# Kernel optimization log

Hardware: AMD Instinct MI355X
Metric: run time of the kernel (lower is better)

## Reference

```python
import jax, jax.numpy as jnp
import numpy as np

D = 128; H = 8; DH = D // H
N = 50000; B = 8; MAXN = N // B
E = 400000
NG_G = 4; NG_L = 4; NG = NG_G + NG_L
DFF = 2 * D


def _ln(x, eps=1e-5):
    m = x.mean(-1, keepdims=True)
    v = ((x - m) ** 2).mean(-1, keepdims=True)
    return (x - m) * jax.lax.rsqrt(v + eps)


def _mha(q, k, v, in_w, in_b, out_w, out_b):
    # torch nn.MultiheadAttention (batch_first, eval) with packed in_proj
    Bq, Lq, d = q.shape; Lk = k.shape[1]
    wq, wk, wv = jnp.split(in_w, 3, axis=0)
    bq, bk, bv = jnp.split(in_b, 3)
    Q = (q @ wq.T + bq).reshape(Bq, Lq, H, DH).transpose(0, 2, 1, 3)
    K = (k @ wk.T + bk).reshape(Bq, Lk, H, DH).transpose(0, 2, 1, 3)
    V = (v @ wv.T + bv).reshape(Bq, Lk, H, DH).transpose(0, 2, 1, 3)
    A = jax.nn.softmax(jnp.einsum('bhqd,bhkd->bhqk', Q, K) / np.float32(np.sqrt(DH)), axis=-1)
    O = jnp.einsum('bhqk,bhkd->bhqd', A, V).transpose(0, 2, 1, 3).reshape(Bq, Lq, d)
    return O @ out_w.T + out_b, A.mean(axis=1)  # averaged attn weights over heads


def _tconv(x, src, dst, Wq, bq, Wk, bk, Wv, bv, Wskip, bskip, Wbeta):
    # PyG TransformerConv(d, d//H, heads=H, beta=True): edge-wise gather-attend-scatter
    n = x.shape[0]
    q = (x @ Wq.T + bq)[dst].reshape(-1, H, DH)   # [E,H,DH] query at target node
    k = (x @ Wk.T + bk)[src].reshape(-1, H, DH)
    v = (x @ Wv.T + bv)[src].reshape(-1, H, DH)
    logits = (q * k).sum(-1) / np.float32(np.sqrt(DH))  # [E,H]
    m = jax.ops.segment_max(logits, dst, num_segments=n)
    m = jnp.where(jnp.isfinite(m), m, 0.0)
    a = jnp.exp(logits - m[dst])
    s = jax.ops.segment_sum(a, dst, num_segments=n)
    alpha = a / (s[dst] + 1e-16)                  # per-target-node softmax (PyG softmax)
    out = jax.ops.segment_sum(v * alpha[..., None], dst, num_segments=n).reshape(n, D)
    xr = x @ Wskip.T + bskip                      # root weight
    beta = jax.nn.sigmoid(jnp.concatenate([out, xr, out - xr], axis=-1) @ Wbeta.T)
    return beta * xr + (1.0 - beta) * out


def setup_inputs() -> dict:
    key = jax.random.key(0)
    ks = jax.random.split(key, 16)
    w = lambda i, shape, s=0.05: jax.random.normal(ks[i], shape, jnp.float32) * s
    return dict(
        x=w(0, (N, D), 1.0),
        edge_index=jax.random.randint(ks[1], (2, E), 0, N),
        global_h=w(2, (B, NG, D), 1.0),
        batch=jnp.repeat(jnp.arange(B, dtype=jnp.int32), MAXN),  # sorted, even split
        n_global_tokens_global=NG_G,
        n_global_tokens_local=NG_L,
        Wq=w(3, (D, D)), bq=jnp.zeros((D,), jnp.float32),
        Wk=w(4, (D, D)), bk=jnp.zeros((D,), jnp.float32),
        Wv=w(5, (D, D)), bv=jnp.zeros((D,), jnp.float32),
        Wskip=w(6, (D, D)), bskip=jnp.zeros((D,), jnp.float32),
        Wbeta=w(7, (1, 3 * D)),
        ng_in_w=w(8, (3 * D, D)), ng_in_b=jnp.zeros((3 * D,), jnp.float32),
        ng_out_w=w(9, (D, D)), ng_out_b=jnp.zeros((D,), jnp.float32),
        gn_in_w=w(10, (3 * D, D)), gn_in_b=jnp.zeros((3 * D,), jnp.float32),
        gn_out_w=w(11, (D, D)), gn_out_b=jnp.zeros((D,), jnp.float32),
        W1=w(12, (DFF, D)), b1=jnp.zeros((DFF,), jnp.float32),
        W2=w(13, (D, DFF)), b2=jnp.zeros((D,), jnp.float32),
    )


def reference(x, edge_index, global_h, batch, n_global_tokens_global, n_global_tokens_local,
              Wq, bq, Wk, bk, Wv, bv, Wskip, bskip, Wbeta,
              ng_in_w, ng_in_b, ng_out_w, ng_out_b,
              gn_in_w, gn_in_b, gn_out_w, gn_out_b,
              W1, b1, W2, b2):
    src, dst = edge_index[0], edge_index[1]
    h_local = _tconv(x, src, dst, Wq, bq, Wk, bk, Wv, bv, Wskip, bskip, Wbeta)
    x = _ln(x + h_local)
    Bg = global_h.shape[0]
    # to_dense_batch: batch is sorted with equal-size graphs -> mask all True, pure reshape
    dense_x = x.reshape(Bg, -1, D)
    global_out, attn_w = _mha(global_h, dense_x, dense_x, ng_in_w, ng_in_b, ng_out_w, ng_out_b)
    global_h = _ln(global_h + global_out)
    nodes_out, _ = _mha(dense_x, global_h, global_h, gn_in_w, gn_in_b, gn_out_w, gn_out_b)
    dense_x = _ln(dense_x + nodes_out)
    x = dense_x.reshape(-1, D)  # un-scatter (even split -> reshape)
    ff = jax.nn.relu(x @ W1.T + b1) @ W2.T + b2
    x = _ln(x + ff)
    # attention regularization, vectorized over the per-graph python loop
    ls = n_global_tokens_global
    le = ls + n_global_tokens_local
    P = attn_w[:, ls:le, :]                      # [B, K, max_n], all nodes valid
    Pn = P / (P.sum(-1, keepdims=True) + 1e-8)
    G = jnp.einsum('bkn,bmn->bkm', Pn, Pn)       # [B, K, K]
    Kt = le - ls
    off = (G.sum(axis=(1, 2)) - jnp.einsum('bkk->b', G)) / (Kt * Kt - Kt)
    reg = off.mean()
    return x, global_h, reg
```

## Files before the change

kernel.cpp:

```cpp
#include <hip/hip_runtime.h>
#include <math.h>

#define D 128
#define H 8
#define NGT 8
#define LSTOK 4
#define NCH 4

typedef short bf16x8 __attribute__((ext_vector_type(8)));
typedef float f32x4  __attribute__((ext_vector_type(4)));

__device__ __forceinline__ short f2bf(float f) {
  union { float f; unsigned u; } v; v.f = f;
  unsigned r = v.u + 0x7FFFu + ((v.u >> 16) & 1u);
  return (short)(r >> 16);
}
__device__ __forceinline__ float bf2f(short s) {
  union { unsigned u; float f; } v;
  v.u = ((unsigned)(unsigned short)s) << 16;
  return v.f;
}
__device__ __forceinline__ float4 bf4(bf16x8 v, int lo) {
  return make_float4(bf2f(v[lo]), bf2f(v[lo + 1]), bf2f(v[lo + 2]), bf2f(v[lo + 3]));
}
__device__ __forceinline__ unsigned pk2(float a, float b) {
  return ((unsigned)(unsigned short)f2bf(b) << 16) | (unsigned short)f2bf(a);
}

__device__ __forceinline__ float dot4(float4 a, float4 b) {
  return a.x*b.x + a.y*b.y + a.z*b.z + a.w*b.w;
}
__device__ __forceinline__ float4 scale_madd(float4 a, float sc, float4 v, float p) {
  return make_float4(fmaf(p, v.x, a.x*sc), fmaf(p, v.y, a.y*sc),
                     fmaf(p, v.z, a.z*sc), fmaf(p, v.w, a.w*sc));
}
__device__ __forceinline__ float4 comb4(float4 a, float e1, float4 c, float e2) {
  return make_float4(a.x*e1 + c.x*e2, a.y*e1 + c.y*e2, a.z*e1 + c.z*e2, a.w*e1 + c.w*e2);
}
__device__ __forceinline__ float4 shfl_xor4(float4 v, int off) {
  return make_float4(__shfl_xor(v.x, off), __shfl_xor(v.y, off),
                     __shfl_xor(v.z, off), __shfl_xor(v.w, off));
}

struct CvtArgs {
  const float* s[10];
  short*       d[10];
  int          n[10];
};

__global__ void cvt_weights(CvtArgs a) {
  int which = blockIdx.y;
  const float* s = a.s[which];
  short* d = a.d[which];
  int n = a.n[which];
  int i = (blockIdx.x * 256 + threadIdx.x) * 4;
  if (i + 3 < n) {
    float4 v = *(const float4*)(s + i);
    d[i]     = f2bf(v.x);
    d[i + 1] = f2bf(v.y);
    d[i + 2] = f2bf(v.z);
    d[i + 3] = f2bf(v.w);
  }
}

__global__ void cvt_x(const float* __restrict__ s, short* __restrict__ d, int n) {
  int i = (blockIdx.x * 256 + threadIdx.x) * 8;
  if (i + 7 < n) {
    float4 a = *(const float4*)(s + i);
    float4 b = *(const float4*)(s + i + 4);
    bf16x8 v;
    v[0] = f2bf(a.x); v[1] = f2bf(a.y); v[2] = f2bf(a.z); v[3] = f2bf(a.w);
    v[4] = f2bf(b.x); v[5] = f2bf(b.y); v[6] = f2bf(b.z); v[7] = f2bf(b.w);
    *(bf16x8*)(d + i) = v;
  }
}

__global__ void concat_bias4(const float* __restrict__ b0, const float* __restrict__ b1,
                             const float* __restrict__ b2, const float* __restrict__ b3,
                             float* __restrict__ out) {
  int t = threadIdx.x;
  out[t] = b0[t]; out[128 + t] = b1[t]; out[256 + t] = b2[t]; out[384 + t] = b3[t];
}

#define EPST 72
template<int K>
__global__ void __launch_bounds__(256) gemm_direct(const short* __restrict__ A,
    const short* __restrict__ Wb, const float* __restrict__ bias,
    short* __restrict__ out16, int C16, int s16,
    float* __restrict__ out32, int s32,
    int Nrows, int Ccols, int relu)
{
  __shared__ short eplds[4][64 * EPST];
  const int t = threadIdx.x;
  const int wid = t >> 6, lane = t & 63;
  const int rowBase = blockIdx.x * 128 + (wid >> 1) * 64;
  const int colBase = blockIdx.y * 128 + (wid & 1) * 64;
  const int lrow = lane & 15;
  const int lk = (lane >> 4) * 8;

  f32x4 acc[4][4];
  f32x4 z4 = {0.f, 0.f, 0.f, 0.f};
#pragma unroll
  for (int m = 0; m < 4; m++)
#pragma unroll
    for (int n = 0; n < 4; n++) acc[m][n] = z4;

  const short* ap[4];
#pragma unroll
  for (int m = 0; m < 4; ++m) {
    int ar = rowBase + m * 16 + lrow;
    if (ar >= Nrows) ar = Nrows - 1;
    ap[m] = A + (size_t)ar * K + lk;
  }
  const short* wp[4];
#pragma unroll
  for (int n = 0; n < 4; ++n)
    wp[n] = Wb + (size_t)(colBase + n * 16 + lrow) * K + lk;

#pragma unroll
  for (int kb = 0; kb < K; kb += 32) {
    bf16x8 af[4], bfr[4];
#pragma unroll
    for (int m = 0; m < 4; ++m) af[m] = *(const bf16x8*)(ap[m] + kb);
#pragma unroll
    for (int n = 0; n < 4; ++n) bfr[n] = *(const bf16x8*)(wp[n] + kb);
#pragma unroll
    for (int m = 0; m < 4; ++m)
#pragma unroll
      for (int n = 0; n < 4; ++n)
        acc[m][n] = __builtin_amdgcn_mfma_f32_16x16x32_bf16(af[m], bfr[n], acc[m][n], 0, 0, 0);
  }

  const int ccol = lane & 15;
  const int rquad = (lane >> 4) * 4;
  if (colBase < C16) {
    short* lds = eplds[wid];
#pragma unroll
    for (int n = 0; n < 4; ++n) {
      float bb = bias[colBase + n * 16 + ccol];
      int col = n * 16 + ccol;
#pragma unroll
      for (int m = 0; m < 4; ++m) {
        int r0 = m * 16 + rquad;
#pragma unroll
        for (int r = 0; r < 4; ++r) {
          float v = acc[m][n][r] + bb;
          if (relu) v = fmaxf(v, 0.f);
          lds[(r0 + r) * EPST + col] = f2bf(v);
        }
      }
    }
    const int jr = lane >> 3, jc = lane & 7;
#pragma unroll
    for (int i = 0; i < 8; ++i) {
      int row = i * 8 + jr;
      int gr = rowBase + row;
      if (gr < Nrows) {
        bf16x8 v = *(const bf16x8*)(lds + row * EPST + jc * 8);
        *(bf16x8*)(out16 + (size_t)gr * s16 + colBase + jc * 8) = v;
      }
    }
  } else {
#pragma unroll
    for (int n = 0; n < 4; ++n) {
      int col = colBase + n * 16 + ccol;
      float bb = bias[col];
#pragma unroll
      for (int m = 0; m < 4; ++m) {
        int row0 = rowBase + m * 16 + rquad;
#pragma unroll
        for (int r = 0; r < 4; ++r) {
          int gr = row0 + r;
          if (gr < Nrows) {
            float v = acc[m][n][r] + bb;
            if (relu) v = fmaxf(v, 0.f);
            out32[(size_t)gr * s32 + (col - C16)] = v;
          }
        }
      }
    }
  }
}

__global__ void gemm_small(const float* __restrict__ A, const float* __restrict__ W,
                           const float* __restrict__ bias, float* __restrict__ out, int M)
{
  int r = blockIdx.x;
  int c = threadIdx.x;
  __shared__ float as[128];
  as[c] = A[(size_t)r * 128 + c];
  __syncthreads();
  float acc = bias[c];
  const float* wr = W + (size_t)c * 128;
#pragma unroll 4
  for (int k = 0; k < 128; k++) acc += as[k] * wr[k];
  out[(size_t)r * 128 + c] = acc;
}

__global__ void count_deg(const int* __restrict__ dst, int* __restrict__ deg, int E) {
  int e = blockIdx.x * 256 + threadIdx.x;
  if (e < E) atomicAdd(&deg[dst[e]], 1);
}

__global__ void scan_pass1(const int* __restrict__ deg, int* __restrict__ bsum, int N) {
  int t = threadIdx.x, lane = t & 63, wid = t >> 6;
  int idx = blockIdx.x * 1024 + t * 4;
  int4 v = {0, 0, 0, 0};
  if (idx + 3 < N) v = *(const int4*)(deg + idx);
  else {
    if (idx < N) v.x = deg[idx];
    if (idx + 1 < N) v.y = deg[idx + 1];
    if (idx + 2 < N) v.z = deg[idx + 2];
    if (idx + 3 < N) v.w = deg[idx + 3];
  }
  int s = v.x + v.y + v.z + v.w;
#pragma unroll
  for (int off = 32; off >= 1; off >>= 1) s += __shfl_xor(s, off);
  __shared__ int ws[4];
  if (lane == 0) ws[wid] = s;
  __syncthreads();
  if (t == 0) bsum[blockIdx.x] = ws[0] + ws[1] + ws[2] + ws[3];
}

__global__ void scan_pass2(int* __restrict__ bsum, int SB) {
  __shared__ int sh[1024];
  int t = threadIdx.x;
  sh[t] = (t < SB) ? bsum[t] : 0;
  __syncthreads();
  for (int off = 1; off < 1024; off <<= 1) {
    int v = (t >= off) ? sh[t - off] : 0;
    __syncthreads();
    sh[t] += v;
    __syncthreads();
  }
  if (t < SB) bsum[t] = (t == 0) ? 0 : sh[t - 1];
}

__global__ void scan_pass3(const int* __restrict__ deg, const int* __restrict__ bsum,
                           int* __restrict__ row_start, int* __restrict__ cursor,
                           int N, int E)
{
  int t = threadIdx.x, lane = t & 63, wid = t >> 6;
  int idx = blockIdx.x * 1024 + t * 4;
  int4 v = {0, 0, 0, 0};
  if (idx + 3 < N) v = *(const int4*)(deg + idx);
  else {
    if (idx < N) v.x = deg[idx];
    if (idx + 1 < N) v.y = deg[idx + 1];
    if (idx + 2 < N) v.z = deg[idx + 2];
    if (idx + 3 < N) v.w = deg[idx + 3];
  }
  int ts = v.x + v.y + v.z + v.w;
  int x = ts;
#pragma unroll
  for (int off = 1; off < 64; off <<= 1) {
    int y = __shfl_up(x, off);
    if (lane >= off) x += y;
  }
  __shared__ int ws[4];
  if (lane == 63) ws[wid] = x;
  __syncthreads();
  int woff = 0;
  for (int i = 0; i < wid; i++) woff += ws[i];
  int p = bsum[blockIdx.x] + woff + (x - ts);
  if (idx < N)     { row_start[idx] = p; cursor[idx] = p; }     p += v.x;
  if (idx + 1 < N) { row_start[idx + 1] = p; cursor[idx + 1] = p; } p += v.y;
  if (idx + 2 < N) { row_start[idx + 2] = p; cursor[idx + 2] = p; } p += v.z;
  if (idx + 3 < N) { row_start[idx + 3] = p; cursor[idx + 3] = p; }
  if (blockIdx.x == 0 && t == 0) row_start[N] = E;
}

__global__ void fill_edges(const int* __restrict__ dst, const int* __restrict__ src,
                           int* __restrict__ cursor, int* __restrict__ edge_src, int E) {
  int e = blockIdx.x * 256 + threadIdx.x;
  if (e < E) {
    int p = atomicAdd(&cursor[dst[e]], 1);
    edge_src[p] = src[e];
  }
}

__global__ void tconv_attn(const short* __restrict__ qkvb,
                           const int* __restrict__ row_start,
                           const int* __restrict__ edge_src,
                           float* __restrict__ out, int N)
{
  int gid = blockIdx.x * 256 + threadIdx.x;
  if (gid >= N * H) return;
  int n = gid >> 3, h = gid & 7;
  const short* qp = qkvb + (size_t)n * 384 + h * 16;
  bf16x8 qa = *(const bf16x8*)(qp);
  bf16x8 qb = *(const bf16x8*)(qp + 8);
  float4 q0 = bf4(qa, 0), q1 = bf4(qa, 4), q2 = bf4(qb, 0), q3 = bf4(qb, 4);
  int e0 = row_start[n], e1 = row_start[n + 1];

  float mA = -3.0e38f, sA = 0.f;
  float4 A0 = make_float4(0, 0, 0, 0), A1 = A0, A2 = A0, A3 = A0;
  float mB = -3.0e38f, sB = 0.f;
  float4 B0 = A0, B1 = A0, B2 = A0, B3 = A0;

  int ei = e0;
  for (; ei + 1 < e1; ei += 2) {
    int sn0 = edge_src[ei], sn1 = edge_src[ei + 1];
    const short* kp0 = qkvb + (size_t)sn0 * 384 + 128 + h * 16;
    const short* kp1 = qkvb + (size_t)sn1 * 384 + 128 + h * 16;
    bf16x8 k00 = *(const bf16x8*)(kp0);
    bf16x8 k01 = *(const bf16x8*)(kp0 + 8);
    bf16x8 k10 = *(const bf16x8*)(kp1);
    bf16x8 k11 = *(const bf16x8*)(kp1 + 8);
    float d0 = (dot4(q0, bf4(k00, 0)) + dot4(q1, bf4(k00, 4))
              + dot4(q2, bf4(k01, 0)) + dot4(q3, bf4(k01, 4))) * 0.25f;
    float d1 = (dot4(q0, bf4(k10, 0)) + dot4(q1, bf4(k10, 4))
              + dot4(q2, bf4(k11, 0)) + dot4(q3, bf4(k11, 4))) * 0.25f;
    bf16x8 v00 = *(const bf16x8*)(kp0 + 128);
    bf16x8 v01 = *(const bf16x8*)(kp0 + 136);
    bf16x8 v10 = *(const bf16x8*)(kp1 + 128);
    bf16x8 v11 = *(const bf16x8*)(kp1 + 136);
    float mn0 = fmaxf(mA, d0);
    float sc0 = expf(mA - mn0), p0 = expf(d0 - mn0);
    A0 = scale_madd(A0, sc0, bf4(v00, 0), p0);
    A1 = scale_madd(A1, sc0, bf4(v00, 4), p0);
    A2 = scale_madd(A2, sc0, bf4(v01, 0), p0);
    A3 = scale_madd(A3, sc0, bf4(v01, 4), p0);
    sA = sA * sc0 + p0; mA = mn0;
    float mn1 = fmaxf(mB, d1);
    float sc1 = expf(mB - mn1), p1 = expf(d1 - mn1);
    B0 = scale_madd(B0, sc1, bf4(v10, 0), p1);
    B1 = scale_madd(B1, sc1, bf4(v10, 4), p1);
    B2 = scale_madd(B2, sc1, bf4(v11, 0), p1);
    B3 = scale_madd(B3, sc1, bf4(v11, 4), p1);
    sB = sB * sc1 + p1; mB = mn1;
  }
  if (ei < e1) {
    int sn0 = edge_src[ei];
    const short* kp0 = qkvb + (size_t)sn0 * 384 + 128 + h * 16;
    bf16x8 k00 = *(const bf16x8*)(kp0);
    bf16x8 k01 = *(const bf16x8*)(kp0 + 8);
    float d0 = (dot4(q0, bf4(k00, 0)) + dot4(q1, bf4(k00, 4))
              + dot4(q2, bf4(k01, 0)) + dot4(q3, bf4(k01, 4))) * 0.25f;
    bf16x8 v00 = *(const bf16x8*)(kp0 + 128);
    bf16x8 v01 = *(const bf16x8*)(kp0 + 136);
    float mn0 = fmaxf(mA, d0);
    float sc0 = expf(mA - mn0), p0 = expf(d0 - mn0);
    A0 = scale_madd(A0, sc0, bf4(v00, 0), p0);
    A1 = scale_madd(A1, sc0, bf4(v00, 4), p0);
    A2 = scale_madd(A2, sc0, bf4(v01, 0), p0);
    A3 = scale_madd(A3, sc0, bf4(v01, 4), p0);
    sA = sA * sc0 + p0; mA = mn0;
  }
  float mn = fmaxf(mA, mB);
  float eA = expf(mA - mn), eB = expf(mB - mn);
  float s = sA * eA + sB * eB;
  float4 a0 = comb4(A0, eA, B0, eB);
  float4 a1 = comb4(A1, eA, B1, eB);
  float4 a2 = comb4(A2, eA, B2, eB);
  float4 a3 = comb4(A3, eA, B3, eB);
  float inv = 1.f / (s + 1e-16f);
  float4* o4 = (float4*)(out + (size_t)n * 128 + h * 16);
  o4[0] = make_float4(a0.x * inv, a0.y * inv, a0.z * inv, a0.w * inv);
  o4[1] = make_float4(a1.x * inv, a1.y * inv, a1.z * inv, a1.w * inv);
  o4[2] = make_float4(a2.x * inv, a2.y * inv, a2.z * inv, a2.w * inv);
  o4[3] = make_float4(a3.x * inv, a3.y * inv, a3.z * inv, a3.w * inv);
}

__global__ void gate_ln(const float* __restrict__ x, const float* __restrict__ att,
                        const float* __restrict__ xr32, const float* __restrict__ Wb,
                        float* __restrict__ x1, short* __restrict__ x1b, int N)
{
  int wid = threadIdx.x >> 6, lane = threadIdx.x & 63;
  int n = blockIdx.x * 4 + wid;
  if (n >= N) return;
  size_t base = (size_t)n * 128 + lane * 2;
  float2 o = *(const float2*)(att + base);
  float2 r = *(const float2*)(xr32 + base);
  float2 xv = *(const float2*)(x + base);
  float2 w0 = *(const float2*)(Wb + lane * 2);
  float2 w1 = *(const float2*)(Wb + 128 + lane * 2);
  float2 w2 = *(const float2*)(Wb + 256 + lane * 2);
  float ts = o.x * w0.x + o.y * w0.y + r.x * w1.x + r.y * w1.y
           + (o.x - r.x) * w2.x + (o.y - r.y) * w2.y;
#pragma unroll
  for (int mm = 32; mm >= 1; mm >>= 1) ts += __shfl_xor(ts, mm);
  float beta = 1.f / (1.f + expf(-ts));
  float2 y;
  y.x = xv.x + beta * r.x + (1.f - beta) * o.x;
  y.y = xv.y + beta * r.y + (1.f - beta) * o.y;
  float sm = y.x + y.y;
#pragma unroll
  for (int mm = 32; mm >= 1; mm >>= 1) sm += __shfl_xor(sm, mm);
  float mean = sm * (1.f / 128.f);
  float dx = y.x - mean, dy = y.y - mean;
  float vs = dx * dx + dy * dy;
#pragma unroll
  for (int mm = 32; mm >= 1; mm >>= 1) vs += __shfl_xor(vs, mm);
  float rstd = rsqrtf(vs * (1.f / 128.f) + 1e-5f);
  float ox = dx * rstd, oy = dy * rstd;
  *(float2*)(x1 + base) = make_float2(ox, oy);
  *(unsigned*)(x1b + base) = pk2(ox, oy);
}

__global__ void ln_add(const float* __restrict__ a, const float* __restrict__ b,
                       float* __restrict__ out, short* __restrict__ out16, int R)
{
  int wid = threadIdx.x >> 6, lane = threadIdx.x & 63;
  int r = blockIdx.x * 4 + wid;
  if (r >= R) return;
  size_t base = (size_t)r * 128 + lane * 2;
  float2 av = *(const float2*)(a + base);
  float2 bv = *(const float2*)(b + base);
  float2 y = make_float2(av.x + bv.x, av.y + bv.y);
  float sm = y.x + y.y;
#pragma unroll
  for (int mm = 32; mm >= 1; mm >>= 1) sm += __shfl_xor(sm, mm);
  float mean = sm * (1.f / 128.f);
  float dx = y.x - mean, dy = y.y - mean;
  float vs = dx * dx + dy * dy;
#pragma unroll
  for (int mm = 32; mm >= 1; mm >>= 1) vs += __shfl_xor(vs, mm);
  float rstd = rsqrtf(vs * (1.f / 128.f) + 1e-5f);
  float ox = dx * rstd, oy = dy * rstd;
  *(float2*)(out + base) = make_float2(ox, oy);
  if (out16) *(unsigned*)(out16 + base) = pk2(ox, oy);
}

__global__ void glob_part(const float* __restrict__ Qg, const short* __restrict__ kv,
                          float* __restrict__ Plog,
                          float* __restrict__ pm, float* __restrict__ ps,
                          float* __restrict__ pacc, int MAXN)
{
  int blk = blockIdx.x;
  int ch = blockIdx.y;
  int h = blk & 7, g = (blk >> 3) & 7, b = blk >> 6;
  int lane = threadIdx.x;
  const float4* q4 = (const float4*)(Qg + (size_t)(b * NGT + g) * 128 + h * 16);
  float4 q0 = q4[0], q1 = q4[1], q2 = q4[2], q3 = q4[3];
  int chunk = (MAXN + NCH - 1) / NCH;
  int n0 = ch * chunk;
  int n1 = n0 + chunk; if (n1 > MAXN) n1 = MAXN;
  float* plrow = (g >= LSTOK) ? Plog + (((size_t)(b * 4 + g - LSTOK)) * H + h) * MAXN : nullptr;
  float m = -3.0e38f, s = 0.f;
  float4 a0 = make_float4(0, 0, 0, 0), a1 = a0, a2 = a0, a3 = a0;
  for (int n = n0 + lane; n < n1; n += 64) {
    const short* kp = kv + ((size_t)(b * MAXN + n)) * 256 + h * 16;
    bf16x8 k0 = *(const bf16x8*)(kp);
    bf16x8 k1 = *(const bf16x8*)(kp + 8);
    float d = dot4(q0, bf4(k0, 0)) + dot4(q1, bf4(k0, 4))
            + dot4(q2, bf4(k1, 0)) + dot4(q3, bf4(k1, 4));
    d *= 0.25f;
    if (plrow) plrow[n] = d;
    float mn = fmaxf(m, d);
    float sc = expf(m - mn);
    float p = expf(d - mn);
    bf16x8 v0 = *(const bf16x8*)(kp + 128);
    bf16x8 v1 = *(const bf16x8*)(kp + 136);
    a0 = scale_madd(a0, sc, bf4(v0, 0), p);
    a1 = scale_madd(a1, sc, bf4(v0, 4), p);
    a2 = scale_madd(a2, sc, bf4(v1, 0), p);
    a3 = scale_madd(a3, sc, bf4(v1, 4), p);
    s = s * sc + p;
    m = mn;
  }
#pragma unroll
  for (int off = 32; off >= 1; off >>= 1) {
    float m2 = __shfl_xor(m, off);
    float s2 = __shfl_xor(s, off);
    float4 c0 = shfl_xor4(a0, off), c1 = shfl_xor4(a1, off);
    float4 c2 = shfl_xor4(a2, off), c3 = shfl_xor4(a3, off);
    float mn = fmaxf(m, m2);
    float e1 = expf(m - mn), e2 = expf(m2 - mn);
    s = s * e1 + s2 * e2;
    a0 = comb4(a0, e1, c0, e2);
    a1 = comb4(a1, e1, c1, e2);
    a2 = comb4(a2, e1, c2, e2);
    a3 = comb4(a3, e1, c3, e2);
    m = mn;
  }
  if (lane == 0) {
    int pi = blk * NCH + ch;
    pm[pi] = m; ps[pi] = s;
    float4* pa = (float4*)(pacc + (size_t)pi * 16);
    pa[0] = a0; pa[1] = a1; pa[2] = a2; pa[3] = a3;
  }
}

__global__ void glob_merge(const float* __restrict__ pm, const float* __restrict__ ps,
                           const float* __restrict__ pacc, float* __restrict__ Og,
                           float* __restrict__ m_gl, float* __restrict__ is_gl)
{
  int blk = blockIdx.x;
  int lane = threadIdx.x;
  float m = -3.0e38f;
#pragma unroll
  for (int c = 0; c < NCH; ++c) m = fmaxf(m, pm[blk * NCH + c]);
  float s = 0.f;
#pragma unroll
  for (int c = 0; c < NCH; ++c) s += ps[blk * NCH + c] * expf(pm[blk * NCH + c] - m);
  if (lane < 16) {
    float a = 0.f;
#pragma unroll
    for (int c = 0; c < NCH; ++c)
      a += pacc[(size_t)(blk * NCH + c) * 16 + lane] * expf(pm[blk * NCH + c] - m);
    int h = blk & 7, g = (blk >> 3) & 7, b = blk >> 6;
    Og[(size_t)(b * NGT + g) * 128 + h * 16 + lane] = a / s;
  }
  if (lane == 0) { m_gl[blk] = m; is_gl[blk] = 1.f / s; }
}

__global__ void pker2(const float* __restrict__ Plog,
                      const float* __restrict__ m_gl, const float* __restrict__ is_gl,
                      float* __restrict__ P, int MAXN)
{
  int b = blockIdx.y;
  __shared__ float ms[32], iss[32];
  if (threadIdx.x < 32) {
    int g = threadIdx.x >> 3, h = threadIdx.x & 7;
    ms[threadIdx.x]  = m_gl[(b * NGT + LSTOK + g) * H + h];
    iss[threadIdx.x] = is_gl[(b * NGT + LSTOK + g) * H + h];
  }
  __syncthreads();
  int n = blockIdx.x * 256 + threadIdx.x;
  if (n >= MAXN) return;
#pragma unroll
  for (int g = 0; g < 4; g++) {
    float acc = 0.f;
#pragma unroll
    for (int h = 0; h < H; h++) {
      float l = Plog[(((size_t)(b * 4 + g)) * H + h) * MAXN + n];
      acc += expf(l - ms[g * 8 + h]) * iss[g * 8 + h];
    }
    P[(size_t)(b * 4 + g) * MAXN + n] = acc * 0.125f;
  }
}

__global__ void regk(const float* __restrict__ P, float* __restrict__ offb, int MAXN)
{
  int b = blockIdx.x;
  int t = threadIdx.x;
  float v[10];
#pragma unroll
  for (int i = 0; i < 10; i++) v[i] = 0.f;
  for (int n = t; n < MAXN; n += 256) {
    float p0 = P[(size_t)(b * 4 + 0) * MAXN + n];
    float p1 = P[(size_t)(b * 4 + 1) * MAXN + n];
    float p2 = P[(size_t)(b * 4 + 2) * MAXN + n];
    float p3 = P[(size_t)(b * 4 + 3) * MAXN + n];
    v[0] += p0; v[1] += p1; v[2] += p2; v[3] += p3;
    v[4] += p0 * p1; v[5] += p0 * p2; v[6] += p0 * p3;
    v[7] += p1 * p2; v[8] += p1 * p3; v[9] += p2 * p3;
  }
#pragma unroll
  for (int i = 0; i < 10; i++) {
    float x = v[i];
#pragma unroll
    for (int mm = 32; mm >= 1; mm >>= 1) x += __shfl_xor(x, mm);
    v[i] = x;
  }
  __shared__ float red[4][10];
  int wid = t >> 6, lane = t & 63;
  if (lane == 0)
    for (int i = 0; i < 10; i++) red[wid][i] = v[i];
  __syncthreads();
  if (t == 0) {
    float r[10];
    for (int i = 0; i < 10; i++) r[i] = red[0][i] + red[1][i] + red[2][i] + red[3][i];
    float r0 = r[0] + 1e-8f, r1 = r[1] + 1e-8f, r2 = r[2] + 1e-8f, r3 = r[3] + 1e-8f;
    float off = 2.f * (r[4] / (r0 * r1) + r[5] / (r0 * r2) + r[6] / (r0 * r3)
                     + r[7] / (r1 * r2) + r[8] / (r1 * r3) + r[9] / (r2 * r3));
    offb[b] = off * (1.f / 12.f);
  }
}

__global__ void regfin(const float* __restrict__ offb, float* __restrict__ out) {
  if (threadIdx.x == 0 && blockIdx.x == 0) {
    float s = 0.f;
    for (int i = 0; i < 8; i++) s += offb[i];
    *out = s * (1.f / 8.f);
  }
}

__global__ void node_attn(const short* __restrict__ Qn, const float* __restrict__ Kg,
                          const float* __restrict__ Vg, short* __restrict__ On,
                          int N, int MAXN)
{
  __shared__ float kg[2][NGT * 128];
  __shared__ float vg[2][NGT * 128];
  int n0 = blockIdx.x * 32;
  int b0 = n0 / MAXN;
  int nlast = n0 + 31; if (nlast >= N) nlast = N - 1;
  int bLast = nlast / MAXN;
  int nb = (bLast != b0) ? 2 : 1;
  for (int bi = 0; bi < nb; ++bi) {
    size_t gb = (size_t)((b0 + bi) * NGT) * 128;
    int i = threadIdx.x * 4;
    *(float4*)&kg[bi][i] = *(const float4*)(Kg + gb + i);
    *(float4*)&vg[bi][i] = *(const float4*)(Vg + gb + i);
  }
  __syncthreads();
  int n = n0 + (threadIdx.x >> 3), h = threadIdx.x & 7;
  if (n >= N) return;
  int bi = (n / MAXN) - b0;
  const short* qp = Qn + (size_t)n * 128 + h * 16;
  bf16x8 qa = *(const bf16x8*)(qp);
  bf16x8 qb = *(const bf16x8*)(qp + 8);
  float4 q0 = bf4(qa, 0), q1 = bf4(qa, 4), q2 = bf4(qb, 0), q3 = bf4(qb, 4);
  float l[NGT];
  float mx = -3.0e38f;
#pragma unroll
  for (int tk = 0; tk < NGT; tk++) {
    const float4* k4 = (const float4*)(&kg[bi][tk * 128 + h * 16]);
    float d = dot4(q0, k4[0]) + dot4(q1, k4[1]) + dot4(q2, k4[2]) + dot4(q3, k4[3]);
    l[tk] = d * 0.25f;
    mx = fmaxf(mx, l[tk]);
  }
  float s = 0.f;
#pragma unroll
  for (int tk = 0; tk < NGT; tk++) { l[tk] = expf(l[tk] - mx); s += l[tk]; }
  float inv = 1.f / s;
  float4 a0 = make_float4(0, 0, 0, 0), a1 = a0, a2 = a0, a3 = a0;
#pragma unroll
  for (int tk = 0; tk < NGT; tk++) {
    float p = l[tk] * inv;
    const float4* v4 = (const float4*)(&vg[bi][tk * 128 + h * 16]);
    a0 = scale_madd(a0, 1.f, v4[0], p);
    a1 = scale_madd(a1, 1.f, v4[1], p);
    a2 = scale_madd(a2, 1.f, v4[2], p);
    a3 = scale_madd(a3, 1.f, v4[3], p);
  }
  unsigned* o = (unsigned*)(On + (size_t)n * 128 + h * 16);
  o[0] = pk2(a0.x, a0.y); o[1] = pk2(a0.z, a0.w);
  o[2] = pk2(a1.x, a1.y); o[3] = pk2(a1.z, a1.w);
  o[4] = pk2(a2.x, a2.y); o[5] = pk2(a2.z, a2.w);
  o[6] = pk2(a3.x, a3.y); o[7] = pk2(a3.z, a3.w);
}

extern "C" void kernel_launch(void* const* d_in, const int* in_sizes, int n_in,
                              void* d_out, int out_size, void* d_ws, size_t ws_size,
                              hipStream_t stream)
{
  const float* x     = (const float*)d_in[0];
  const int*   ei    = (const int*)d_in[1];
  const float* gh    = (const float*)d_in[2];
  const float* Wq    = (const float*)d_in[6];
  const float* bqv   = (const float*)d_in[7];
  const float* Wk    = (const float*)d_in[8];
  const float* bkv   = (const float*)d_in[9];
  const float* Wv    = (const float*)d_in[10];
  const float* bvv   = (const float*)d_in[11];
  const float* Wsk   = (const float*)d_in[12];
  const float* bsk   = (const float*)d_in[13];
  const float* Wbeta = (const float*)d_in[14];
  const float* ngw   = (const float*)d_in[15];
  const float* ngb   = (const float*)d_in[16];
  const float* ngow  = (const float*)d_in[17];
  const float* ngob  = (const float*)d_in[18];
  const float* gnw   = (const float*)d_in[19];
  const float* gnb   = (const float*)d_in[20];
  const float* gnow  = (const float*)d_in[21];
  const float* gnob  = (const float*)d_in[22];
  const float* W1    = (const float*)d_in[23];
  const float* b1v   = (const float*)d_in[24];
  const float* W2    = (const float*)d_in[25];
  const float* b2v   = (const float*)d_in[26];

  const int N    = in_sizes[0] / D;
  const int E    = in_sizes[1] / 2;
  const int Bb   = 8;
  const int MAXN = N / Bb;

  const int* srcI = ei;
  const int* dstI = ei + E;

  size_t NF = (size_t)N;
  size_t ND = NF * D;
  float* fw = (float*)d_ws;
  short* qkvb = (short*)fw;
  short* kv16 = qkvb;
  short* ff1b = qkvb;
  float* xr32 = fw + NF * 192;
  short* Qnb  = (short*)xr32;
  short* Onb  = (short*)(xr32 + NF * 64);
  float* ff2o = xr32;
  float* x1   = fw + NF * 320;
  short* x1b  = (short*)(fw + NF * 448);
  float* misc = fw + NF * 512;
  float* Qg    = misc;
  float* Og    = Qg + 8192;
  float* gout  = Og + 8192;
  float* Kg    = gout + 8192;
  float* Vg    = Kg + 8192;
  float* m_gl  = Vg + 8192;
  float* is_gl = m_gl + 512;
  float* Pbuf  = is_gl + 512;
  float* offb  = Pbuf + (size_t)Bb * 4 * MAXN;
  float* bias512 = offb + 16;
  float* Plog  = bias512 + 512;
  float* pm    = Plog + (size_t)4 * H * Bb * MAXN;
  float* ps    = pm + 512 * NCH;
  float* pacc  = ps + 512 * NCH;
  int* deg       = (int*)(pacc + 512 * NCH * 16);
  int* row_start = deg + N;
  int* cursor    = row_start + N + 1;
  int* bsum      = cursor + N;
  int* edge_src  = bsum + 1024;
  short* wbase = (short*)((((uintptr_t)(edge_src + E)) + 15) & ~(uintptr_t)15);
  short* cWq  = wbase;
  short* cWk  = cWq  + 16384;
  short* cWv  = cWk  + 16384;
  short* cWsk = cWv  + 16384;
  short* cNgK = cWsk + 16384;
  short* cNgV = cNgK + 16384;
  short* cGnQ = cNgV + 16384;
  short* cGnO = cGnQ + 16384;
  short* cW1  = cGnO + 16384;
  short* cW2  = cW1  + 32768;
  short* xb   = cW2  + 32768;

  float* outx   = (float*)d_out;
  float* outgh  = outx + ND;
  float* outreg = outgh + (size_t)Bb * NGT * D;
  float* wa     = outx;

  const int GXM = (N + 127) / 128;
  const int SB  = (N + 1023) / 1024;
  dim3 blk256(256);

  CvtArgs ca;
  ca.s[0] = Wq;   ca.d[0] = cWq;  ca.n[0] = 16384;
  ca.s[1] = Wk;   ca.d[1] = cWk;  ca.n[1] = 16384;
  ca.s[2] = Wv;   ca.d[2] = cWv;  ca.n[2] = 16384;
  ca.s[3] = Wsk;  ca.d[3] = cWsk; ca.n[3] = 16384;
  ca.s[4] = ngw + 128 * 128; ca.d[4] = cNgK; ca.n[4] = 16384;
  ca.s[5] = ngw + 256 * 128; ca.d[5] = cNgV; ca.n[5] = 16384;
  ca.s[6] = gnw;  ca.d[6] = cGnQ; ca.n[6] = 16384;
  ca.s[7] = gnow; ca.d[7] = cGnO; ca.n[7] = 16384;
  ca.s[8] = W1;   ca.d[8] = cW1;  ca.n[8] = 32768;
  ca.s[9] = W2;   ca.d[9] = cW2;  ca.n[9] = 32768;
  cvt_weights<<<dim3(32, 10), blk256, 0, stream>>>(ca);
  concat_bias4<<<dim3(1), dim3(128), 0, stream>>>(bqv, bkv, bvv, bsk, bias512);
  cvt_x<<<dim3((N * 128 / 8 + 255) / 256), blk256, 0, stream>>>(x, xb, N * 128);

  hipMemsetAsync(deg, 0, (size_t)N * sizeof(int), stream);
  count_deg<<<dim3((E + 255) / 256), blk256, 0, stream>>>(dstI, deg, E);
  scan_pass1<<<dim3(SB), blk256, 0, stream>>>(deg, bsum, N);
  scan_pass2<<<dim3(1), dim3(1024), 0, stream>>>(bsum, SB);
  scan_pass3<<<dim3(SB), blk256, 0, stream>>>(deg, bsum, row_start, cursor, N, E);
  fill_edges<<<dim3((E + 255) / 256), blk256, 0, stream>>>(dstI, srcI, cursor, edge_src, E);

  gemm_direct<128><<<dim3(GXM, 4), blk256, 0, stream>>>(xb, cWq, bias512,
                                                        qkvb, 384, 384, xr32, 128,
                                                        N, 512, 0);

  tconv_attn<<<dim3((N * H + 255) / 256), blk256, 0, stream>>>(qkvb, row_start, edge_src, wa, N);
  gate_ln<<<dim3((N + 3) / 4), blk256, 0, stream>>>(x, wa, xr32, Wbeta, x1, x1b, N);

  gemm_direct<128><<<dim3(GXM, 2), blk256, 0, stream>>>(x1b, cNgK, ngb + 128,
                                                        kv16, 256, 256, nullptr, 0,
                                                        N, 256, 0);
  gemm_small<<<dim3(64), dim3(128), 0, stream>>>(gh, ngw, ngb, Qg, 64);
  glob_part<<<dim3(512, NCH), dim3(64), 0, stream>>>(Qg, kv16, Plog, pm, ps, pacc, MAXN);
  glob_merge<<<dim3(512), dim3(64), 0, stream>>>(pm, ps, pacc, Og, m_gl, is_gl);
  pker2<<<dim3((MAXN + 255) / 256, 8), blk256, 0, stream>>>(Plog, m_gl, is_gl, Pbuf, MAXN);
  regk<<<dim3(8), blk256, 0, stream>>>(Pbuf, offb, MAXN);
  regfin<<<dim3(1), dim3(64), 0, stream>>>(offb, outreg);

  gemm_small<<<dim3(64), dim3(128), 0, stream>>>(Og, ngow, ngob, gout, 64);
  ln_add<<<dim3(16), blk256, 0, stream>>>(gh, gout, outgh, nullptr, 64);

  gemm_small<<<dim3(64), dim3(128), 0, stream>>>(outgh, gnw + 128 * 128, gnb + 128, Kg, 64);
  gemm_small<<<dim3(64), dim3(128), 0, stream>>>(outgh, gnw + 256 * 128, gnb + 256, Vg, 64);
  gemm_direct<128><<<dim3(GXM, 1), blk256, 0, stream>>>(x1b, cGnQ, gnb,
                                                        Qnb, 128, 128, nullptr, 0,
                                                        N, 128, 0);
  node_attn<<<dim3((N + 31) / 32), blk256, 0, stream>>>(Qnb, Kg, Vg, Onb, N, MAXN);
  gemm_direct<128><<<dim3(GXM, 1), blk256, 0, stream>>>(Onb, cGnO, gnob,
                                                        nullptr, 0, 0, wa, 128,
                                                        N, 128, 0);
  ln_add<<<dim3((N + 3) / 4), blk256, 0, stream>>>(x1, wa, x1, x1b, N);

  gemm_direct<128><<<dim3(GXM, 2), blk256, 0, stream>>>(x1b, cW1, b1v,
                                                        ff1b, 256, 256, nullptr, 0,
                                                        N, 256, 1);
  gemm_direct<256><<<dim3(GXM, 1), blk256, 0, stream>>>(ff1b, cW2, b2v,
                                                        nullptr, 0, 0, ff2o, 128,
                                                        N, 128, 0);
  ln_add<<<dim3((N + 3) / 4), blk256, 0, stream>>>(x1, ff2o, outx, nullptr, N);
}
```

Before: 394.6 us.

## Fuse FFN GEMMs and node-attention pipeline into single LDS-staged kernels

Adds gemm_ff, which computes the relu hidden layer of the feed-forward block into shared memory as bf16 and runs the second GEMM from there, so the 256-wide intermediate never goes to global memory. Adds gemm_node, which fuses the Q projection, the per-node attention over the 8 global tokens, and the output projection in one kernel with Q and the attention output held in LDS. The QKV GEMM now writes the skip projection as bf16 in a 512-wide packed buffer, and gate_ln reads it from there instead of a separate fp32 buffer. Together these cut launches and global round-trips, at the cost of large LDS use per block (about 66 KB in gemm_ff), which lowers occupancy, and bf16 rounding of the skip term.

New measurement: 361.3 us, median of 2. 8.4% less time.

```diff
diff --git a/kernel.cpp b/kernel.cpp
--- a/kernel.cpp
+++ b/kernel.cpp
@@ -182,6 +182,276 @@
   }
 }
 
+#define FFST 264
+__global__ void __launch_bounds__(256) gemm_ff(const short* __restrict__ A,
+    const short* __restrict__ W1b, const float* __restrict__ b1,
+    const short* __restrict__ W2b, const float* __restrict__ b2,
+    float* __restrict__ out, int Nrows)
+{
+  __shared__ short flds[128 * FFST];
+  const int t = threadIdx.x;
+  const int wid = t >> 6, lane = t & 63;
+  const int rowL = (wid >> 1) * 64;
+  const int rowBase = blockIdx.x * 128 + rowL;
+  const int lrow = lane & 15;
+  const int lk = (lane >> 4) * 8;
+  const int ccol = lane & 15;
+  const int rquad = (lane >> 4) * 4;
+  f32x4 z4 = {0.f, 0.f, 0.f, 0.f};
+
+  const short* ap[4];
+#pragma unroll
+  for (int m = 0; m < 4; ++m) {
+    int ar = rowBase + m * 16 + lrow;
+    if (ar >= Nrows) ar = Nrows - 1;
+    ap[m] = A + (size_t)ar * 128 + lk;
+  }
+
+  for (int cb = 0; cb < 2; ++cb) {
+    int colBase = cb * 128 + (wid & 1) * 64;
+    f32x4 acc[4][4];
+#pragma unroll
+    for (int m = 0; m < 4; m++)
+#pragma unroll
+      for (int n = 0; n < 4; n++) acc[m][n] = z4;
+    const short* wp[4];
+#pragma unroll
+    for (int n = 0; n < 4; ++n)
+      wp[n] = W1b + (size_t)(colBase + n * 16 + lrow) * 128 + lk;
+#pragma unroll
+    for (int kb = 0; kb < 128; kb += 32) {
+      bf16x8 af[4], bfr[4];
+#pragma unroll
+      for (int m = 0; m < 4; ++m) af[m] = *(const bf16x8*)(ap[m] + kb);
+#pragma unroll
+      for (int n = 0; n < 4; ++n) bfr[n] = *(const bf16x8*)(wp[n] + kb);
+#pragma unroll
+      for (int m = 0; m < 4; ++m)
+#pragma unroll
+        for (int n = 0; n < 4; ++n)
+          acc[m][n] = __builtin_amdgcn_mfma_f32_16x16x32_bf16(af[m], bfr[n], acc[m][n], 0, 0, 0);
+    }
+#pragma unroll
+    for (int n = 0; n < 4; ++n) {
+      int col = colBase + n * 16 + ccol;
+      float bb = b1[col];
+#pragma unroll
+      for (int m = 0; m < 4; ++m) {
+        int r0 = rowL + m * 16 + rquad;
+#pragma unroll
+        for (int r = 0; r < 4; ++r) {
+          float v = fmaxf(acc[m][n][r] + bb, 0.f);
+          flds[(r0 + r) * FFST + col] = f2bf(v);
+        }
+      }
+    }
+  }
+  __syncthreads();
+
+  {
+    int colBase = (wid & 1) * 64;
+    f32x4 acc[4][4];
+#pragma unroll
+    for (int m = 0; m < 4; m++)
+#pragma unroll
+      for (int n = 0; n < 4; n++) acc[m][n] = z4;
+    const short* wp[4];
+#pragma unroll
+    for (int n = 0; n < 4; ++n)
+      wp[n] = W2b + (size_t)(colBase + n * 16 + lrow) * 256 + lk;
+#pragma unroll
+    for (int kb = 0; kb < 256; kb += 32) {
+      bf16x8 af[4], bfr[4];
+#pragma unroll
+      for (int m = 0; m < 4; ++m)
+        af[m] = *(const bf16x8*)(flds + (rowL + m * 16 + lrow) * FFST + kb + lk);
+#pragma unroll
+      for (int n = 0; n < 4; ++n) bfr[n] = *(const bf16x8*)(wp[n] + kb);
+#pragma unroll
+      for (int m = 0; m < 4; ++m)
+#pragma unroll
+        for (int n = 0; n < 4; ++n)
+          acc[m][n] = __builtin_amdgcn_mfma_f32_16x16x32_bf16(af[m], bfr[n], acc[m][n], 0, 0, 0);
+    }
+#pragma unroll
+    for (int n = 0; n < 4; ++n) {
+      int col = colBase + n * 16 + ccol;
+      float bb = b2[col];
+#pragma unroll
+      for (int m = 0; m < 4; ++m) {
+        int row0 = rowBase + m * 16 + rquad;
+#pragma unroll
+        for (int r = 0; r < 4; ++r) {
+          int gr = row0 + r;
+          if (gr < Nrows) out[(size_t)gr * 128 + col] = acc[m][n][r] + bb;
+        }
+      }
+    }
+  }
+}
+
+#define QST 136
+__global__ void __launch_bounds__(256) gemm_node(const short* __restrict__ A,
+    const short* __restrict__ GnQb, const float* __restrict__ gnbq,
+    const float* __restrict__ Kg, const float* __restrict__ Vg,
+    const short* __restrict__ GnOb, const float* __restrict__ gnbo,
+    float* __restrict__ out, int Nrows, int MAXN)
+{
+  __shared__ short qlds[128 * QST];
+  __shared__ float kg[2][NGT * 128];
+  __shared__ float vg[2][NGT * 128];
+  const int t = threadIdx.x;
+  const int wid = t >> 6, lane = t & 63;
+  const int rowL = (wid >> 1) * 64;
+  const int n0 = blockIdx.x * 128;
+  const int rowBase = n0 + rowL;
+  const int colBase = (wid & 1) * 64;
+  const int lrow = lane & 15;
+  const int lk = (lane >> 4) * 8;
+  const int ccol = lane & 15;
+  const int rquad = (lane >> 4) * 4;
+  f32x4 z4 = {0.f, 0.f, 0.f, 0.f};
+
+  int b0 = n0 / MAXN;
+  int nlast = n0 + 127; if (nlast >= Nrows) nlast = Nrows - 1;
+  int bLast = nlast / MAXN;
+  int nb = (bLast != b0) ? 2 : 1;
+  for (int bi = 0; bi < nb; ++bi) {
+    size_t gb = (size_t)((b0 + bi) * NGT) * 128;
+    int i = t * 4;
+    *(float4*)&kg[bi][i] = *(const float4*)(Kg + gb + i);
+    *(float4*)&vg[bi][i] = *(const float4*)(Vg + gb + i);
+  }
+
+  {
+    f32x4 acc[4][4];
+#pragma unroll
+    for (int m = 0; m < 4; m++)
+#pragma unroll
+      for (int n = 0; n < 4; n++) acc[m][n] = z4;
+    const short* ap[4];
+#pragma unroll
+    for (int m = 0; m < 4; ++m) {
+      int ar = rowBase + m * 16 + lrow;
+      if (ar >= Nrows) ar = Nrows - 1;
+      ap[m] = A + (size_t)ar * 128 + lk;
+    }
+    const short* wp[4];
+#pragma unroll
+    for (int n = 0; n < 4; ++n)
+      wp[n] = GnQb + (size_t)(colBase + n * 16 + lrow) * 128 + lk;
+#pragma unroll
+    for (int kb = 0; kb < 128; kb += 32) {
+      bf16x8 af[4], bfr[4];
+#pragma unroll
+      for (int m = 0; m < 4; ++m) af[m] = *(const bf16x8*)(ap[m] + kb);
+#pragma unroll
+      for (int n = 0; n < 4; ++n) bfr[n] = *(const bf16x8*)(wp[n] + kb);
+#pragma unroll
+      for (int m = 0; m < 4; ++m)
+#pragma unroll
+        for (int n = 0; n < 4; ++n)
+          acc[m][n] = __builtin_amdgcn_mfma_f32_16x16x32_bf16(af[m], bfr[n], acc[m][n], 0, 0, 0);
+    }
+#pragma unroll
+    for (int n = 0; n < 4; ++n) {
+      int col = colBase + n * 16 + ccol;
+      float bb = gnbq[col];
+#pragma unroll
+      for (int m = 0; m < 4; ++m) {
+        int r0 = rowL + m * 16 + rquad;
+#pragma unroll
+        for (int r = 0; r < 4; ++r)
+          qlds[(r0 + r) * QST + col] = f2bf(acc[m][n][r] + bb);
+      }
+    }
+  }
+  __syncthreads();
+
+#pragma unroll
+  for (int u = 0; u < 4; ++u) {
+    int unit = t + u * 256;
+    int row = unit >> 3, h = unit & 7;
+    int grow = n0 + row;
+    if (grow < Nrows) {
+      int bi = (grow / MAXN) - b0;
+      short* qp = qlds + row * QST + h * 16;
+      bf16x8 qa = *(const bf16x8*)(qp);
+      bf16x8 qb = *(const bf16x8*)(qp + 8);
+      float4 q0 = bf4(qa, 0), q1 = bf4(qa, 4), q2 = bf4(qb, 0), q3 = bf4(qb, 4);
+      float l[NGT];
+      float mx = -3.0e38f;
+#pragma unroll
+      for (int tk = 0; tk < NGT; tk++) {
+        const float4* k4 = (const float4*)(&kg[bi][tk * 128 + h * 16]);
+        float d = dot4(q0, k4[0]) + dot4(q1, k4[1]) + dot4(q2, k4[2]) + dot4(q3, k4[3]);
+        l[tk] = d * 0.25f;
+        mx = fmaxf(mx, l[tk]);
+      }
+      float s = 0.f;
+#pragma unroll
+      for (int tk = 0; tk < NGT; tk++) { l[tk] = expf(l[tk] - mx); s += l[tk]; }
+      float inv = 1.f / s;
+      float4 a0 = make_float4(0, 0, 0, 0), a1 = a0, a2 = a0, a3 = a0;
+#pragma unroll
+      for (int tk = 0; tk < NGT; tk++) {
+        float p = l[tk] * inv;
+        const float4* v4 = (const float4*)(&vg[bi][tk * 128 + h * 16]);
+        a0 = scale_madd(a0, 1.f, v4[0], p);
+        a1 = scale_madd(a1, 1.f, v4[1], p);
+        a2 = scale_madd(a2, 1.f, v4[2], p);
+        a3 = scale_madd(a3, 1.f, v4[3], p);
+      }
+      unsigned* o = (unsigned*)qp;
+      o[0] = pk2(a0.x, a0.y); o[1] = pk2(a0.z, a0.w);
+      o[2] = pk2(a1.x, a1.y); o[3] = pk2(a1.z, a1.w);
+      o[4] = pk2(a2.x, a2.y); o[5] = pk2(a2.z, a2.w);
+      o[6] = pk2(a3.x, a3.y); o[7] = pk2(a3.z, a3.w);
+    }
+  }
+  __syncthreads();
+
+  {
+    f32x4 acc[4][4];
+#pragma unroll
+    for (int m = 0; m < 4; m++)
+#pragma unroll
+      for (int n = 0; n < 4; n++) acc[m][n] = z4;
+    const short* wp[4];
+#pragma unroll
+    for (int n = 0; n < 4; ++n)
+      wp[n] = GnOb + (size_t)(colBase + n * 16 + lrow) * 128 + lk;
+#pragma unroll
+    for (int kb = 0; kb < 128; kb += 32) {
+      bf16x8 af[4], bfr[4];
+#pragma unroll
+      for (int m = 0; m < 4; ++m)
+        af[m] = *(const bf16x8*)(qlds + (rowL + m * 16 + lrow) * QST + kb + lk);
+#pragma unroll
+      for (int n = 0; n < 4; ++n) bfr[n] = *(const bf16x8*)(wp[n] + kb);
+#pragma unroll
+      for (int m = 0; m < 4; ++m)
+#pragma unroll
+        for (int n = 0; n < 4; ++n)
+          acc[m][n] = __builtin_amdgcn_mfma_f32_16x16x32_bf16(af[m], bfr[n], acc[m][n], 0, 0, 0);
+    }
+#pragma unroll
+    for (int n = 0; n < 4; ++n) {
+      int col = colBase + n * 16 + ccol;
+      float bb = gnbo[col];
+#pragma unroll
+      for (int m = 0; m < 4; ++m) {
+        int row0 = rowBase + m * 16 + rquad;
+#pragma unroll
+        for (int r = 0; r < 4; ++r) {
+          int gr = row0 + r;
+          if (gr < Nrows) out[(size_t)gr * 128 + col] = acc[m][n][r] + bb;
+        }
+      }
+    }
+  }
+}
+
 __global__ void gemm_small(const float* __restrict__ A, const float* __restrict__ W,
                            const float* __restrict__ bias, float* __restrict__ out, int M)
 {
@@ -287,7 +557,7 @@
   int gid = blockIdx.x * 256 + threadIdx.x;
   if (gid >= N * H) return;
   int n = gid >> 3, h = gid & 7;
-  const short* qp = qkvb + (size_t)n * 384 + h * 16;
+  const short* qp = qkvb + (size_t)n * 512 + h * 16;
   bf16x8 qa = *(const bf16x8*)(qp);
   bf16x8 qb = *(const bf16x8*)(qp + 8);
   float4 q0 = bf4(qa, 0), q1 = bf4(qa, 4), q2 = bf4(qb, 0), q3 = bf4(qb, 4);
@@ -301,8 +571,8 @@
   int ei = e0;
   for (; ei + 1 < e1; ei += 2) {
     int sn0 = edge_src[ei], sn1 = edge_src[ei + 1];
-    const short* kp0 = qkvb + (size_t)sn0 * 384 + 128 + h * 16;
-    const short* kp1 = qkvb + (size_t)sn1 * 384 + 128 + h * 16;
+    const short* kp0 = qkvb + (size_t)sn0 * 512 + 128 + h * 16;
+    const short* kp1 = qkvb + (size_t)sn1 * 512 + 128 + h * 16;
     bf16x8 k00 = *(const bf16x8*)(kp0);
     bf16x8 k01 = *(const bf16x8*)(kp0 + 8);
     bf16x8 k10 = *(const bf16x8*)(kp1);
@@ -332,7 +602,7 @@
   }
   if (ei < e1) {
     int sn0 = edge_src[ei];
-    const short* kp0 = qkvb + (size_t)sn0 * 384 + 128 + h * 16;
+    const short* kp0 = qkvb + (size_t)sn0 * 512 + 128 + h * 16;
     bf16x8 k00 = *(const bf16x8*)(kp0);
     bf16x8 k01 = *(const bf16x8*)(kp0 + 8);
     float d0 = (dot4(q0, bf4(k00, 0)) + dot4(q1, bf4(k00, 4))
@@ -363,7 +633,7 @@
 }
 
 __global__ void gate_ln(const float* __restrict__ x, const float* __restrict__ att,
-                        const float* __restrict__ xr32, const float* __restrict__ Wb,
+                        const short* __restrict__ qkvb, const float* __restrict__ Wb,
                         float* __restrict__ x1, short* __restrict__ x1b, int N)
 {
   int wid = threadIdx.x >> 6, lane = threadIdx.x & 63;
@@ -371,7 +641,8 @@
   if (n >= N) return;
   size_t base = (size_t)n * 128 + lane * 2;
   float2 o = *(const float2*)(att + base);
-  float2 r = *(const float2*)(xr32 + base);
+  unsigned ru = *(const unsigned*)(qkvb + (size_t)n * 512 + 384 + lane * 2);
+  float2 r = make_float2(bf2f((short)(ru & 0xFFFF)), bf2f((short)(ru >> 16)));
   float2 xv = *(const float2*)(x + base);
   float2 w0 = *(const float2*)(Wb + lane * 2);
   float2 w1 = *(const float2*)(Wb + 128 + lane * 2);
@@ -577,61 +848,6 @@
   }
 }
 
-__global__ void node_attn(const short* __restrict__ Qn, const float* __restrict__ Kg,
-                          const float* __restrict__ Vg, short* __restrict__ On,
-                          int N, int MAXN)
-{
-  __shared__ float kg[2][NGT * 128];
-  __shared__ float vg[2][NGT * 128];
-  int n0 = blockIdx.x * 32;
-  int b0 = n0 / MAXN;
-  int nlast = n0 + 31; if (nlast >= N) nlast = N - 1;
-  int bLast = nlast / MAXN;
-  int nb = (bLast != b0) ? 2 : 1;
-  for (int bi = 0; bi < nb; ++bi) {
-    size_t gb = (size_t)((b0 + bi) * NGT) * 128;
-    int i = threadIdx.x * 4;
-    *(float4*)&kg[bi][i] = *(const float4*)(Kg + gb + i);
-    *(float4*)&vg[bi][i] = *(const float4*)(Vg + gb + i);
-  }
-  __syncthreads();
-  int n = n0 + (threadIdx.x >> 3), h = threadIdx.x & 7;
-  if (n >= N) return;
-  int bi = (n / MAXN) - b0;
-  const short* qp = Qn + (size_t)n * 128 + h * 16;
-  bf16x8 qa = *(const bf16x8*)(qp);
-  bf16x8 qb = *(const bf16x8*)(qp + 8);
-  float4 q0 = bf4(qa, 0), q1 = bf4(qa, 4), q2 = bf4(qb, 0), q3 = bf4(qb, 4);
-  float l[NGT];
-  float mx = -3.0e38f;
-#pragma unroll
-  for (int tk = 0; tk < NGT; tk++) {
-    const float4* k4 = (const float4*)(&kg[bi][tk * 128 + h * 16]);
-    float d = dot4(q0, k4[0]) + dot4(q1, k4[1]) + dot4(q2, k4[2]) + dot4(q3, k4[3]);
-    l[tk] = d * 0.25f;
-    mx = fmaxf(mx, l[tk]);
-  }
-  float s = 0.f;
-#pragma unroll
-  for (int tk = 0; tk < NGT; tk++) { l[tk] = expf(l[tk] - mx); s += l[tk]; }
-  float inv = 1.f / s;
-  float4 a0 = make_float4(0, 0, 0, 0), a1 = a0, a2 = a0, a3 = a0;
-#pragma unroll
-  for (int tk = 0; tk < NGT; tk++) {
-    float p = l[tk] * inv;
-    const float4* v4 = (const float4*)(&vg[bi][tk * 128 + h * 16]);
-    a0 = scale_madd(a0, 1.f, v4[0], p);
-    a1 = scale_madd(a1, 1.f, v4[1], p);
-    a2 = scale_madd(a2, 1.f, v4[2], p);
-    a3 = scale_madd(a3, 1.f, v4[3], p);
-  }
-  unsigned* o = (unsigned*)(On + (size_t)n * 128 + h * 16);
-  o[0] = pk2(a0.x, a0.y); o[1] = pk2(a0.z, a0.w);
-  o[2] = pk2(a1.x, a1.y); o[3] = pk2(a1.z, a1.w);
-  o[4] = pk2(a2.x, a2.y); o[5] = pk2(a2.z, a2.w);
-  o[6] = pk2(a3.x, a3.y); o[7] = pk2(a3.z, a3.w);
-}
-
 extern "C" void kernel_launch(void* const* d_in, const int* in_sizes, int n_in,
                               void* d_out, int out_size, void* d_ws, size_t ws_size,
                               hipStream_t stream)
@@ -674,14 +890,10 @@
   float* fw = (float*)d_ws;
   short* qkvb = (short*)fw;
   short* kv16 = qkvb;
-  short* ff1b = qkvb;
-  float* xr32 = fw + NF * 192;
-  short* Qnb  = (short*)xr32;
-  short* Onb  = (short*)(xr32 + NF * 64);
-  float* ff2o = xr32;
-  float* x1   = fw + NF * 320;
-  short* x1b  = (short*)(fw + NF * 448);
-  float* misc = fw + NF * 512;
+  float* ff2o = fw + NF * 256;
+  float* x1   = fw + NF * 384;
+  short* x1b  = (short*)(fw + NF * 512);
+  float* misc = fw + NF * 576;
   float* Qg    = misc;
   float* Og    = Qg + 8192;
   float* gout  = Og + 8192;
@@ -746,11 +958,11 @@
   fill_edges<<<dim3((E + 255) / 256), blk256, 0, stream>>>(dstI, srcI, cursor, edge_src, E);
 
   gemm_direct<128><<<dim3(GXM, 4), blk256, 0, stream>>>(xb, cWq, bias512,
-                                                        qkvb, 384, 384, xr32, 128,
+                                                        qkvb, 512, 512, nullptr, 0,
                                                         N, 512, 0);
 
   tconv_attn<<<dim3((N * H + 255) / 256), blk256, 0, stream>>>(qkvb, row_start, edge_src, wa, N);
-  gate_ln<<<dim3((N + 3) / 4), blk256, 0, stream>>>(x, wa, xr32, Wbeta, x1, x1b, N);
+  gate_ln<<<dim3((N + 3) / 4), blk256, 0, stream>>>(x, wa, qkvb, Wbeta, x1, x1b, N);
 
   gemm_direct<128><<<dim3(GXM, 2), blk256, 0, stream>>>(x1b, cNgK, ngb + 128,
                                                         kv16, 256, 256, nullptr, 0,
@@ -767,20 +979,10 @@
 
   gemm_small<<<dim3(64), dim3(128), 0, stream>>>(outgh, gnw + 128 * 128, gnb + 128, Kg, 64);
   gemm_small<<<dim3(64), dim3(128), 0, stream>>>(outgh, gnw + 256 * 128, gnb + 256, Vg, 64);
-  gemm_direct<128><<<dim3(GXM, 1), blk256, 0, stream>>>(x1b, cGnQ, gnb,
-                                                        Qnb, 128, 128, nullptr, 0,
-                                                        N, 128, 0);
-  node_attn<<<dim3((N + 31) / 32), blk256, 0, stream>>>(Qnb, Kg, Vg, Onb, N, MAXN);
-  gemm_direct<128><<<dim3(GXM, 1), blk256, 0, stream>>>(Onb, cGnO, gnob,
-                                                        nullptr, 0, 0, wa, 128,
-                                                        N, 128, 0);
+  gemm_node<<<dim3(GXM), blk256, 0, stream>>>(x1b, cGnQ, gnb, Kg, Vg, cGnO, gnob,
+                                              wa, N, MAXN);
   ln_add<<<dim3((N + 3) / 4), blk256, 0, stream>>>(x1, wa, x1, x1b, N);
 
-  gemm_direct<128><<<dim3(GXM, 2), blk256, 0, stream>>>(x1b, cW1, b1v,
-                                                        ff1b, 256, 256, nullptr, 0,
-                                                        N, 256, 1);
-  gemm_direct<256><<<dim3(GXM, 1), blk256, 0, stream>>>(ff1b, cW2, b2v,
-                                                        nullptr, 0, 0, ff2o, 128,
-                                                        N, 128, 0);
+  gemm_ff<<<dim3(GXM), blk256, 0, stream>>>(x1b, cW1, b1v, cW2, b2v, ff2o, N);
   ln_add<<<dim3((N + 3) / 4), blk256, 0, stream>>>(x1, ff2o, outx, nullptr, N);
 }
```
